# Optimization experiments

Measured on AMD Instinct MI355X. Metric: run time of the kernel, lower is better.

The kernel has to match this reference:

```python
import jax, jax.numpy as jnp
import numpy as np

N_NODES = 100000
N_EDGES = 3200000
N_GRAPHS = 5000
N_LAYERS = 2
BN_EPS = 1e-5


def setup_inputs() -> dict:
    key = jax.random.key(0)
    ks = jax.random.split(key, 20)
    inp = {}
    inp['x'] = jax.random.normal(ks[0], (N_NODES, 14), dtype=jnp.float32)
    inp['edge_index'] = jax.random.randint(ks[1], (2, N_EDGES), 0, N_NODES, dtype=jnp.int64)
    inp['edge_attr'] = jax.random.uniform(ks[2], (N_EDGES, 3), dtype=jnp.float32)
    inp['batch'] = jnp.sort(jax.random.randint(ks[3], (N_NODES,), 0, N_GRAPHS, dtype=jnp.int64))
    s = 0.1
    inp['node_w'] = jax.random.normal(ks[4], (14, 32), dtype=jnp.float32) * s
    inp['node_b'] = jnp.zeros((32,), dtype=jnp.float32)
    inp['edge_w'] = jax.random.normal(ks[5], (3, 32), dtype=jnp.float32) * s
    inp['edge_b'] = jnp.zeros((32,), dtype=jnp.float32)
    inp['conv_w1'] = jax.random.normal(ks[6], (N_LAYERS, 32, 75), dtype=jnp.float32) * s
    inp['conv_b1'] = jnp.zeros((N_LAYERS, 75), dtype=jnp.float32)
    inp['conv_w2'] = jax.random.normal(ks[7], (N_LAYERS, 75, 32), dtype=jnp.float32) * s
    inp['conv_b2'] = jnp.zeros((N_LAYERS, 32), dtype=jnp.float32)
    inp['bn_g'] = jnp.ones((N_LAYERS, 32), dtype=jnp.float32)
    inp['bn_b'] = jnp.zeros((N_LAYERS, 32), dtype=jnp.float32)
    inp['lin1_w'] = jax.random.normal(ks[8], (32, 16), dtype=jnp.float32) * s
    inp['lin1_b'] = jnp.zeros((16,), dtype=jnp.float32)
    inp['lin2_w'] = jax.random.normal(ks[9], (16, 2), dtype=jnp.float32) * s
    inp['lin2_b'] = jnp.zeros((2,), dtype=jnp.float32)
    return inp


def _forward(x, edge_attr, node_w, node_b, edge_w, edge_b,
             conv_w1, conv_b1, conv_w2, conv_b2, bn_g, bn_b,
             lin1_w, lin1_b, lin2_w, lin2_b, edge_index, batch):
    src, dst = edge_index[0], edge_index[1]
    h = x @ node_w + node_b                      # [N, 32]
    ea = edge_attr @ edge_w + edge_b             # [E, 32]
    for l in range(N_LAYERS):
        # GINEConv (eps=0): nn(x_i + sum_j relu(x_j + e_ji))
        msg = jax.nn.relu(h[src] + ea)           # [E, 32]
        agg = jax.ops.segment_sum(msg, dst, num_segments=N_NODES)
        z = h + agg
        z = jax.nn.relu(z @ conv_w1[l] + conv_b1[l]) @ conv_w2[l] + conv_b2[l]
        # BatchNorm1d (training-mode batch statistics)
        mu = jnp.mean(z, axis=0)
        var = jnp.var(z, axis=0)
        z = (z - mu) * jax.lax.rsqrt(var + BN_EPS) * bn_g[l] + bn_b[l]
        h = jax.nn.relu(z)
    # global_mean_pool
    sums = jax.ops.segment_sum(h, batch, num_segments=N_GRAPHS)   # [G, 32]
    counts = jax.ops.segment_sum(jnp.ones((h.shape[0],), h.dtype), batch, num_segments=N_GRAPHS)
    graph_x = sums / jnp.maximum(counts, 1.0)[:, None]
    pred = jax.nn.relu(graph_x @ lin1_w + lin1_b) @ lin2_w + lin2_b  # [G, 2]
    return pred


def reference(x, edge_index, edge_attr, batch, node_w, node_b, edge_w, edge_b,
              conv_w1, conv_b1, conv_w2, conv_b2, bn_g, bn_b,
              lin1_w, lin1_b, lin2_w, lin2_b):
    return _forward(x, edge_attr, node_w, node_b, edge_w, edge_b,
                    conv_w1, conv_b1, conv_w2, conv_b2, bn_g, bn_b,
                    lin1_w, lin1_b, lin2_w, lin2_b, edge_index, batch)
```

## Files before the change

kernel.cpp:

```cpp
#include <hip/hip_runtime.h>
#include <hip/hip_fp16.h>

#define N_NODES 100000
#define N_EDGES 3200000
#define N_GRAPHS 5000
#define BN_EPS 1e-5f
#define HPAD 80
#define CHUNK 2048
#define NBLKA 1563
#define NBKT 196
#define NPAD2 (NBKT * 512)
#define NS1 1197
#define LALLOC (NS1 * 256)
#define VPT 5
#define W1S 36

__global__ void k_encode(const float* __restrict__ x, const float* __restrict__ W,
                         const float* __restrict__ b, float* __restrict__ h,
                         __half* __restrict__ h16) {
    __shared__ float sW[448];
    __shared__ float sb[32];
    for (int i = threadIdx.x; i < 448; i += 256) sW[i] = W[i];
    if (threadIdx.x < 32) sb[threadIdx.x] = b[threadIdx.x];
    __syncthreads();
    int n = blockIdx.x * 256 + threadIdx.x;
    if (n >= N_NODES) return;
    float xi[14];
#pragma unroll
    for (int k = 0; k < 14; k++) xi[k] = x[n * 14 + k];
    float4* hp = (float4*)(h + (size_t)n * 32);
    __half2* hq = (__half2*)(h16 + (size_t)n * 32);
#pragma unroll
    for (int q = 0; q < 8; q++) {
        float4 acc;
        float* ap = (float*)&acc;
#pragma unroll
        for (int i = 0; i < 4; i++) {
            int c = q * 4 + i;
            float a = sb[c];
#pragma unroll
            for (int k = 0; k < 14; k++) a += xi[k] * sW[k * 32 + c];
            ap[i] = a;
        }
        hp[q] = acc;
        hq[q * 2 + 0] = __floats2half2_rn(acc.x, acc.y);
        hq[q * 2 + 1] = __floats2half2_rn(acc.z, acc.w);
    }
}

__global__ void k_prep(const float* __restrict__ W1, const float* __restrict__ b1,
                       const float* __restrict__ W2,
                       float* __restrict__ w1tp, float* __restrict__ b1p,
                       float* __restrict__ w2p) {
    int i = blockIdx.x * 256 + threadIdx.x;
    if (i < 2 * HPAD * 32) {
        int l = i / (HPAD * 32), r = i % (HPAD * 32);
        int j = r / 32, c = r % 32;
        w1tp[i] = (j < 75) ? W1[l * 2400 + c * 75 + j] : 0.f;
        w2p[i]  = (j < 75) ? W2[l * 2400 + j * 32 + c] : 0.f;
    } else if (i < 2 * HPAD * 32 + 2 * HPAD) {
        int k = i - 2 * HPAD * 32;
        int l = k / HPAD, j = k % HPAD;
        b1p[k] = (j < 75) ? b1[l * 75 + j] : 0.f;
    }
}

__global__ void __launch_bounds__(256) ksA(const int* __restrict__ ei, int* __restrict__ cmat) {
    __shared__ int lh[NBKT];
    if (threadIdx.x < NBKT) lh[threadIdx.x] = 0;
    __syncthreads();
    int b0 = blockIdx.x * CHUNK;
    for (int i = threadIdx.x; i < CHUNK; i += 256) {
        int e = b0 + i;
        if (e < N_EDGES) atomicAdd(&lh[ei[N_EDGES + e] >> 9], 1);
    }
    __syncthreads();
    if (threadIdx.x < NBKT) cmat[threadIdx.x * NBLKA + blockIdx.x] = lh[threadIdx.x];
}

__global__ void ks1(const int* __restrict__ a, int* __restrict__ bs) {
    __shared__ int s[256];
    int i = blockIdx.x * 256 + threadIdx.x;
    s[threadIdx.x] = a[i];
    __syncthreads();
    for (int o = 128; o > 0; o >>= 1) {
        if (threadIdx.x < o) s[threadIdx.x] += s[threadIdx.x + o];
        __syncthreads();
    }
    if (threadIdx.x == 0) bs[blockIdx.x] = s[0];
}

__global__ void ks2(int* __restrict__ bs) {
    __shared__ int s[256];
    int t = threadIdx.x;
    int v[VPT];
    int base = t * VPT, sum = 0;
#pragma unroll
    for (int k = 0; k < VPT; k++) {
        int idx = base + k;
        int x = (idx < NS1) ? bs[idx] : 0;
        v[k] = sum; sum += x;
    }
    s[t] = sum;
    __syncthreads();
    for (int o = 1; o < 256; o <<= 1) {
        int add = (t >= o) ? s[t - o] : 0;
        __syncthreads();
        s[t] += add;
        __syncthreads();
    }
    int excl = (t == 0) ? 0 : s[t - 1];
#pragma unroll
    for (int k = 0; k < VPT; k++) {
        int idx = base + k;
        if (idx < NS1) bs[idx] = excl + v[k];
    }
}

__global__ void ks3(int* __restrict__ a, const int* __restrict__ bs) {
    __shared__ int s[256];
    int t = threadIdx.x, i = blockIdx.x * 256 + t;
    int v = a[i];
    s[t] = v;
    __syncthreads();
    for (int o = 1; o < 256; o <<= 1) {
        int add = (t >= o) ? s[t - o] : 0;
        __syncthreads();
        s[t] += add;
        __syncthreads();
    }
    a[i] = s[t] - v + bs[blockIdx.x];
}

__global__ void __launch_bounds__(256) ksB(const int* __restrict__ ei, const float* __restrict__ ea,
                                           const int* __restrict__ cmat, float4* __restrict__ buf1) {
    __shared__ float4 rec[CHUNK];
    __shared__ unsigned short sbkt[CHUNK];
    __shared__ int lh[NBKT];
    __shared__ int lex[NBKT];
    __shared__ int gb[NBKT];
    __shared__ int sc[256];
    int t = threadIdx.x;
    int b0 = blockIdx.x * CHUNK;
    int nval = min(CHUNK, N_EDGES - b0);
    if (t < NBKT) lh[t] = 0;
    __syncthreads();
    for (int i = t; i < nval; i += 256)
        atomicAdd(&lh[ei[N_EDGES + b0 + i] >> 9], 1);
    __syncthreads();
    sc[t] = (t < NBKT) ? lh[t] : 0;
    __syncthreads();
    for (int o = 1; o < 256; o <<= 1) {
        int add = (t >= o) ? sc[t - o] : 0;
        __syncthreads();
        sc[t] += add;
        __syncthreads();
    }
    if (t < NBKT) {
        lex[t] = sc[t] - lh[t];
        gb[t] = cmat[t * NBLKA + blockIdx.x];
        lh[t] = sc[t] - lh[t];
    }
    __syncthreads();
    for (int i = t; i < nval; i += 256) {
        int e = b0 + i;
        int src = ei[e], dst = ei[N_EDGES + e];
        float a0 = ea[(size_t)e * 3 + 0], a1 = ea[(size_t)e * 3 + 1], a2 = ea[(size_t)e * 3 + 2];
        int bkt = dst >> 9;
        int r = atomicAdd(&lh[bkt], 1);
        rec[r] = make_float4(a0, a1, a2, __int_as_float(src | ((dst & 511) << 17)));
        sbkt[r] = (unsigned short)bkt;
    }
    __syncthreads();
    for (int p = t; p < nval; p += 256) {
        int bkt = sbkt[p];
        buf1[gb[bkt] + (p - lex[bkt])] = rec[p];
    }
}

__global__ void __launch_bounds__(1024) ksC(const int* __restrict__ cmat, const float4* __restrict__ buf1,
                                            float4* __restrict__ packed, int* __restrict__ offs) {
    __shared__ int cnt[512];
    __shared__ int sc[512];
    __shared__ int excl[513];
    int g = blockIdx.x, t = threadIdx.x;
    int bb = cmat[g * NBLKA];
    int be = (g == NBKT - 1) ? N_EDGES : cmat[(g + 1) * NBLKA];
    if (t < 512) cnt[t] = 0;
    __syncthreads();
    for (int j = bb + t; j < be; j += 1024) {
        int bits = __float_as_int(buf1[j].w);
        atomicAdd(&cnt[bits >> 17], 1);
    }
    __syncthreads();
    if (t < 512) sc[t] = cnt[t];
    __syncthreads();
    for (int o = 1; o < 512; o <<= 1) {
        int add = 0;
        if (t < 512 && t >= o) add = sc[t - o];
        __syncthreads();
        if (t < 512) sc[t] += add;
        __syncthreads();
    }
    if (t < 512) excl[t] = sc[t] - cnt[t];
    if (t == 511) excl[512] = sc[511];
    __syncthreads();
    if (t < 512) offs[g * 512 + t] = bb + excl[t];
    if (g == NBKT - 1 && t == 0) offs[NPAD2] = N_EDGES;
    if (t < 512) cnt[t] = 0;
    __syncthreads();
    for (int j = bb + t; j < be; j += 1024) {
        float4 r = buf1[j];
        int bits = __float_as_int(r.w);
        int dl = bits >> 17, src = bits & 0x1FFFF;
        int rank = atomicAdd(&cnt[dl], 1);
        packed[bb + excl[dl] + rank] = make_float4(r.x, r.y, r.z, __int_as_float(src));
    }
}

__global__ void __launch_bounds__(256) k_agg(const float4* __restrict__ packed,
                                             const int* __restrict__ offs,
                                             const float* __restrict__ eW, const float* __restrict__ eb,
                                             const __half* __restrict__ h16,
                                             const float* __restrict__ h, float* __restrict__ zin) {
    int t = blockIdx.x * 256 + threadIdx.x;
    int n = t >> 5, s = t & 31;
    int q = s & 7, part = s >> 3;
    int c0 = q * 4;
    float w0[4], w1[4], w2[4], bb4[4];
#pragma unroll
    for (int i = 0; i < 4; i++) {
        w0[i] = eW[c0 + i];
        w1[i] = eW[32 + c0 + i];
        w2[i] = eW[64 + c0 + i];
        bb4[i] = eb[c0 + i];
    }
    int beg = offs[n], end = offs[n + 1];
    float acc0[4] = {0.f, 0.f, 0.f, 0.f};
    float acc1[4] = {0.f, 0.f, 0.f, 0.f};
    int j = beg + part;
    for (; j + 4 < end; j += 8) {
        float4 pa = packed[j];
        float4 pb = packed[j + 4];
        float2 ra = *(const float2*)(h16 + (size_t)__float_as_int(pa.w) * 32 + c0);
        float2 rb = *(const float2*)(h16 + (size_t)__float_as_int(pb.w) * 32 + c0);
        float2 a01 = __half22float2(*(__half2*)&ra.x);
        float2 a23 = __half22float2(*(__half2*)&ra.y);
        float2 b01 = __half22float2(*(__half2*)&rb.x);
        float2 b23 = __half22float2(*(__half2*)&rb.y);
        float ha4[4] = {a01.x, a01.y, a23.x, a23.y};
        float hb4[4] = {b01.x, b01.y, b23.x, b23.y};
#pragma unroll
        for (int i = 0; i < 4; i++) {
            acc0[i] += fmaxf(ha4[i] + pa.x * w0[i] + pa.y * w1[i] + pa.z * w2[i] + bb4[i], 0.f);
            acc1[i] += fmaxf(hb4[i] + pb.x * w0[i] + pb.y * w1[i] + pb.z * w2[i] + bb4[i], 0.f);
        }
    }
    if (j < end) {
        float4 p = packed[j];
        float2 r = *(const float2*)(h16 + (size_t)__float_as_int(p.w) * 32 + c0);
        float2 a01 = __half22float2(*(__half2*)&r.x);
        float2 a23 = __half22float2(*(__half2*)&r.y);
        float hp4[4] = {a01.x, a01.y, a23.x, a23.y};
#pragma unroll
        for (int i = 0; i < 4; i++)
            acc0[i] += fmaxf(hp4[i] + p.x * w0[i] + p.y * w1[i] + p.z * w2[i] + bb4[i], 0.f);
    }
    float acc[4];
#pragma unroll
    for (int i = 0; i < 4; i++) {
        acc[i] = acc0[i] + acc1[i];
        acc[i] += __shfl_xor(acc[i], 8, 64);
        acc[i] += __shfl_xor(acc[i], 16, 64);
    }
    if (part == 0) {
        float4 hq = *(const float4*)(h + (size_t)n * 32 + c0);
        *(float4*)(zin + (size_t)n * 32 + c0) =
            make_float4(acc[0] + hq.x, acc[1] + hq.y, acc[2] + hq.z, acc[3] + hq.w);
    }
}

__global__ void __launch_bounds__(256, 4) k_mlp(float* __restrict__ zio,
                                                const float* __restrict__ W1, const float* __restrict__ B1,
                                                const float* __restrict__ W2, const float* __restrict__ b2) {
    __shared__ float sW1[HPAD * W1S];
    __shared__ float sW2[2560];
    __shared__ float sB1[80];
    __shared__ float sb2[32];
    __shared__ float hidL[32 * 84];
    for (int i = threadIdx.x; i < 2560; i += 256) {
        int j = i >> 5, c = i & 31;
        sW1[j * W1S + c] = W1[i];
        sW2[i] = W2[i];
    }
    if (threadIdx.x < 80) sB1[threadIdx.x] = B1[threadIdx.x];
    if (threadIdx.x < 32) sb2[threadIdx.x] = b2[threadIdx.x];
    __syncthreads();
    unsigned t = blockIdx.x * 256 + threadIdx.x;
    unsigned lane = threadIdx.x & 63;
    unsigned wv = threadIdx.x >> 6;
    unsigned oct = lane >> 3;
    unsigned nd = lane & 7;
    unsigned n = (t >> 6) * 8 + nd;
    const float4* ap = (const float4*)(zio + (size_t)n * 32);
    float zc[32];
#pragma unroll
    for (int q = 0; q < 8; q++) {
        float4 av = ap[q];
        zc[q * 4 + 0] = av.x;
        zc[q * 4 + 1] = av.y;
        zc[q * 4 + 2] = av.z;
        zc[q * 4 + 3] = av.w;
    }
    float hid[10];
#pragma unroll
    for (int i = 0; i < 10; i++) {
        int j = (int)oct * 10 + i;
        const float4* wp = (const float4*)(sW1 + j * W1S);
        float a0 = 0.f, a1 = 0.f, a2 = 0.f, a3 = 0.f;
#pragma unroll
        for (int q = 0; q < 8; q++) {
            float4 wv4 = wp[q];
            a0 += zc[q * 4 + 0] * wv4.x;
            a1 += zc[q * 4 + 1] * wv4.y;
            a2 += zc[q * 4 + 2] * wv4.z;
            a3 += zc[q * 4 + 3] * wv4.w;
        }
        hid[i] = fmaxf(sB1[j] + ((a0 + a1) + (a2 + a3)), 0.f);
    }
    float* hrow = &hidL[(wv * 8 + nd) * 84];
#pragma unroll
    for (int i = 0; i < 10; i++) hrow[oct * 10 + i] = hid[i];
    float4 zo = *(const float4*)(sb2 + oct * 4);
    const float4* hv4 = (const float4*)hrow;
#pragma unroll
    for (int k = 0; k < 20; k++) {
        float4 hv = hv4[k];
        const float* wr = sW2 + (k * 4) * 32 + oct * 4;
        float4 wa = *(const float4*)(wr);
        float4 wb = *(const float4*)(wr + 32);
        float4 wc = *(const float4*)(wr + 64);
        float4 wd = *(const float4*)(wr + 96);
        zo.x += hv.x * wa.x + hv.y * wb.x + hv.z * wc.x + hv.w * wd.x;
        zo.y += hv.x * wa.y + hv.y * wb.y + hv.z * wc.y + hv.w * wd.y;
        zo.z += hv.x * wa.z + hv.y * wb.z + hv.z * wc.z + hv.w * wd.z;
        zo.w += hv.x * wa.w + hv.y * wb.w + hv.z * wc.w + hv.w * wd.w;
    }
    *(float4*)(zio + (size_t)n * 32 + oct * 4) = zo;
}

__global__ void __launch_bounds__(256) k_stats(const float* __restrict__ z, float* __restrict__ stats) {
    __shared__ float ls[4 * 64];
    int tid = threadIdx.x;
    int c = tid & 31;
    float s = 0.f, s2 = 0.f;
    for (int e = blockIdx.x * 256 + tid; e < N_NODES * 32; e += 256 * 256) {
        float v = z[e];
        s += v; s2 += v * v;
    }
    s += __shfl_down(s, 32, 64);
    s2 += __shfl_down(s2, 32, 64);
    int wave = tid >> 6, lane = tid & 63;
    if (lane < 32) { ls[wave * 64 + c] = s; ls[wave * 64 + 32 + c] = s2; }
    __syncthreads();
    if (tid < 64) {
        float a = ls[tid] + ls[64 + tid] + ls[128 + tid] + ls[192 + tid];
        atomicAdd(&stats[tid], a);
    }
}

__global__ void k_bn(const float* __restrict__ z, float* __restrict__ h,
                     __half* __restrict__ h16,
                     const float* __restrict__ stats, const float* __restrict__ g,
                     const float* __restrict__ b) {
    int t = blockIdx.x * 256 + threadIdx.x;
    if (t >= N_NODES * 8) return;
    int q = t & 7;
    float4 zv = ((const float4*)z)[t];
    float* zp = (float*)&zv;
    float4 ov;
    float* op = (float*)&ov;
    const float invN = 1.0f / (float)N_NODES;
#pragma unroll
    for (int i = 0; i < 4; i++) {
        int c = q * 4 + i;
        float mu = stats[c] * invN;
        float var = stats[32 + c] * invN - mu * mu;
        float sc = g[c] / sqrtf(var + BN_EPS);
        op[i] = fmaxf((zp[i] - mu) * sc + b[c], 0.f);
    }
    ((float4*)h)[t] = ov;
    __half2 p0 = __floats2half2_rn(ov.x, ov.y);
    __half2 p1 = __floats2half2_rn(ov.z, ov.w);
    __half2* hq = (__half2*)(h16 + (size_t)t * 4);
    hq[0] = p0;
    hq[1] = p1;
}

__global__ void k_goff(const int* __restrict__ batch, int* __restrict__ goff) {
    int g = blockIdx.x * 256 + threadIdx.x;
    if (g > N_GRAPHS) return;
    int lo = 0, hi = N_NODES;
    while (lo < hi) {
        int mid = (lo + hi) >> 1;
        if (batch[mid] < g) lo = mid + 1; else hi = mid;
    }
    goff[g] = lo;
}

__global__ void __launch_bounds__(256) k_pool2(const float* __restrict__ h, const int* __restrict__ goff,
                                               float* __restrict__ gsum) {
    int wid = threadIdx.x >> 6, lane = threadIdx.x & 63;
    int g = blockIdx.x * 4 + wid;
    if (g >= N_GRAPHS) return;
    int s = goff[g], e = goff[g + 1];
    int c = lane & 31, half = lane >> 5;
    float acc = 0.f;
    for (int n = s + half; n < e; n += 2) acc += h[(size_t)n * 32 + c];
    acc += __shfl_down(acc, 32, 64);
    if (lane < 32) gsum[(size_t)g * 32 + c] = acc;
}

__global__ void k_head(const float* __restrict__ gsum, const int* __restrict__ goff,
                       const float* __restrict__ W1, const float* __restrict__ b1,
                       const float* __restrict__ W2, const float* __restrict__ b2,
                       float* __restrict__ out) {
    __shared__ float sW1[512], sb1[16], sW2[32], sb2[2];
    for (int i = threadIdx.x; i < 512; i += 256) sW1[i] = W1[i];
    if (threadIdx.x < 16) sb1[threadIdx.x] = b1[threadIdx.x];
    if (threadIdx.x < 32) sW2[threadIdx.x] = W2[threadIdx.x];
    if (threadIdx.x < 2) sb2[threadIdx.x] = b2[threadIdx.x];
    __syncthreads();
    int gI = blockIdx.x * 256 + threadIdx.x;
    if (gI >= N_GRAPHS) return;
    float cnt = (float)(goff[gI + 1] - goff[gI]);
    float inv = 1.0f / fmaxf(cnt, 1.0f);
    float gx[32];
#pragma unroll
    for (int c = 0; c < 32; c++) gx[c] = gsum[(size_t)gI * 32 + c] * inv;
    float hid[16];
#pragma unroll
    for (int j = 0; j < 16; j++) {
        float a = sb1[j];
#pragma unroll
        for (int c = 0; c < 32; c++) a += gx[c] * sW1[c * 16 + j];
        hid[j] = fmaxf(a, 0.f);
    }
#pragma unroll
    for (int o = 0; o < 2; o++) {
        float a = sb2[o];
#pragma unroll
        for (int j = 0; j < 16; j++) a += hid[j] * sW2[j * 2 + o];
        out[(size_t)gI * 2 + o] = a;
    }
}

extern "C" void kernel_launch(void* const* d_in, const int* in_sizes, int n_in,
                              void* d_out, int out_size, void* d_ws, size_t ws_size,
                              hipStream_t stream) {
    const float* x       = (const float*)d_in[0];
    const int*   ei      = (const int*)d_in[1];
    const float* eattr   = (const float*)d_in[2];
    const int*   batch   = (const int*)d_in[3];
    const float* node_w  = (const float*)d_in[4];
    const float* node_b  = (const float*)d_in[5];
    const float* edge_w  = (const float*)d_in[6];
    const float* edge_b  = (const float*)d_in[7];
    const float* conv_w1 = (const float*)d_in[8];
    const float* conv_b1 = (const float*)d_in[9];
    const float* conv_w2 = (const float*)d_in[10];
    const float* conv_b2 = (const float*)d_in[11];
    const float* bn_g    = (const float*)d_in[12];
    const float* bn_b    = (const float*)d_in[13];
    const float* lin1_w  = (const float*)d_in[14];
    const float* lin1_b  = (const float*)d_in[15];
    const float* lin2_w  = (const float*)d_in[16];
    const float* lin2_b  = (const float*)d_in[17];
    float* out = (float*)d_out;

    float4* packed = (float4*)d_ws;
    float4* buf1   = packed + N_EDGES;
    float*  h      = (float*)(buf1 + N_EDGES);
    float*  agg    = h + (size_t)N_NODES * 32;
    __half* h16    = (__half*)(agg + (size_t)N_NODES * 32);
    int*    cmat   = (int*)(h16 + (size_t)N_NODES * 32);
    int*    t1     = cmat + LALLOC;
    int*    offs   = t1 + 1280;
    int*    goff   = offs + NPAD2 + 1;
    float*  stats  = (float*)(goff + N_GRAPHS + 1);
    float*  gsum   = stats + 64;
    float*  w1tp   = gsum + (size_t)N_GRAPHS * 32;
    float*  b1p    = w1tp + 2 * HPAD * 32;
    float*  w2p    = b1p + 2 * HPAD;

    int nb_nodes = (N_NODES + 255) / 256;
    int nb_vec   = (N_NODES * 8 + 255) / 256;

    hipMemsetAsync(cmat, 0, LALLOC * sizeof(int), stream);
    k_encode<<<nb_nodes, 256, 0, stream>>>(x, node_w, node_b, h, h16);
    k_prep<<<(2 * HPAD * 32 + 2 * HPAD + 255) / 256, 256, 0, stream>>>(
        conv_w1, conv_b1, conv_w2, w1tp, b1p, w2p);
    k_goff<<<(N_GRAPHS + 1 + 255) / 256, 256, 0, stream>>>(batch, goff);

    ksA<<<NBLKA, 256, 0, stream>>>(ei, cmat);
    ks1<<<NS1, 256, 0, stream>>>(cmat, t1);
    ks2<<<1, 256, 0, stream>>>(t1);
    ks3<<<NS1, 256, 0, stream>>>(cmat, t1);
    ksB<<<NBLKA, 256, 0, stream>>>(ei, eattr, cmat, buf1);
    ksC<<<NBKT, 1024, 0, stream>>>(cmat, buf1, packed, offs);

    for (int l = 0; l < 2; l++) {
        hipMemsetAsync(stats, 0, 64 * sizeof(float), stream);
        k_agg<<<N_NODES * 32 / 256, 256, 0, stream>>>(packed, offs, edge_w, edge_b, h16, h, agg);
        k_mlp<<<N_NODES * 8 / 256, 256, 0, stream>>>(agg, w1tp + l * HPAD * 32,
                                                     b1p + l * HPAD, w2p + l * HPAD * 32,
                                                     conv_b2 + l * 32);
        k_stats<<<256, 256, 0, stream>>>(agg, stats);
        k_bn<<<nb_vec, 256, 0, stream>>>(agg, h, h16, stats, bn_g + l * 32, bn_b + l * 32);
    }
    k_pool2<<<(N_GRAPHS + 3) / 4, 256, 0, stream>>>(h, goff, gsum);
    k_head<<<(N_GRAPHS + 255) / 256, 256, 0, stream>>>(gsum, goff, lin1_w, lin1_b, lin2_w, lin2_b, out);
}
```

Before: 471.1 us.

## Replace two-level edge sort with coarse buckets and shared-memory atomic aggregation

Switches the destination bucketing from 512-node to 128-node buckets and drops the second-level per-node sort kernel (ksC) and its offsets array. Aggregation now runs one block per bucket, accumulating messages into a padded shared-memory tile with LDS float atomics before adding h and writing out. It also skips the fp16 copy of h after the last layer, since nothing reads it. This removes a full pass over the 3.2M edge records. The cost is atomic contention in shared memory, only 782 aggregation blocks, and a float summation order that is no longer deterministic.

Result: slower. 1.688 ms (+258.2%).

```diff
diff --git a/kernel.cpp b/kernel.cpp
--- a/kernel.cpp
+++ b/kernel.cpp
@@ -8,11 +8,11 @@
 #define HPAD 80
 #define CHUNK 2048
 #define NBLKA 1563
-#define NBKT 196
-#define NPAD2 (NBKT * 512)
-#define NS1 1197
+#define NBKT 782
+#define LROW 33
+#define NS1 4775
 #define LALLOC (NS1 * 256)
-#define VPT 5
+#define VPT 19
 #define W1S 36
 
 __global__ void k_encode(const float* __restrict__ x, const float* __restrict__ W,
@@ -67,15 +67,16 @@
 
 __global__ void __launch_bounds__(256) ksA(const int* __restrict__ ei, int* __restrict__ cmat) {
     __shared__ int lh[NBKT];
-    if (threadIdx.x < NBKT) lh[threadIdx.x] = 0;
+    for (int i = threadIdx.x; i < NBKT; i += 256) lh[i] = 0;
     __syncthreads();
     int b0 = blockIdx.x * CHUNK;
     for (int i = threadIdx.x; i < CHUNK; i += 256) {
         int e = b0 + i;
-        if (e < N_EDGES) atomicAdd(&lh[ei[N_EDGES + e] >> 9], 1);
-    }
-    __syncthreads();
-    if (threadIdx.x < NBKT) cmat[threadIdx.x * NBLKA + blockIdx.x] = lh[threadIdx.x];
+        if (e < N_EDGES) atomicAdd(&lh[ei[N_EDGES + e] >> 7], 1);
+    }
+    __syncthreads();
+    for (int i = threadIdx.x; i < NBKT; i += 256)
+        cmat[i * NBLKA + blockIdx.x] = lh[i];
 }
 
 __global__ void ks1(const int* __restrict__ a, int* __restrict__ bs) {
@@ -143,12 +144,19 @@
     int t = threadIdx.x;
     int b0 = blockIdx.x * CHUNK;
     int nval = min(CHUNK, N_EDGES - b0);
-    if (t < NBKT) lh[t] = 0;
+    for (int i = t; i < NBKT; i += 256) lh[i] = 0;
     __syncthreads();
     for (int i = t; i < nval; i += 256)
-        atomicAdd(&lh[ei[N_EDGES + b0 + i] >> 9], 1);
-    __syncthreads();
-    sc[t] = (t < NBKT) ? lh[t] : 0;
+        atomicAdd(&lh[ei[N_EDGES + b0 + i] >> 7], 1);
+    __syncthreads();
+    int v[4]; int run = 0;
+#pragma unroll
+    for (int k = 0; k < 4; k++) {
+        int idx = t * 4 + k;
+        int x = (idx < NBKT) ? lh[idx] : 0;
+        v[k] = run; run += x;
+    }
+    sc[t] = run;
     __syncthreads();
     for (int o = 1; o < 256; o <<= 1) {
         int add = (t >= o) ? sc[t - o] : 0;
@@ -156,19 +164,25 @@
         sc[t] += add;
         __syncthreads();
     }
-    if (t < NBKT) {
-        lex[t] = sc[t] - lh[t];
-        gb[t] = cmat[t * NBLKA + blockIdx.x];
-        lh[t] = sc[t] - lh[t];
+    int excl = (t == 0) ? 0 : sc[t - 1];
+#pragma unroll
+    for (int k = 0; k < 4; k++) {
+        int idx = t * 4 + k;
+        if (idx < NBKT) {
+            int base = excl + v[k];
+            lex[idx] = base;
+            lh[idx] = base;
+            gb[idx] = cmat[idx * NBLKA + blockIdx.x];
+        }
     }
     __syncthreads();
     for (int i = t; i < nval; i += 256) {
         int e = b0 + i;
         int src = ei[e], dst = ei[N_EDGES + e];
         float a0 = ea[(size_t)e * 3 + 0], a1 = ea[(size_t)e * 3 + 1], a2 = ea[(size_t)e * 3 + 2];
-        int bkt = dst >> 9;
+        int bkt = dst >> 7;
         int r = atomicAdd(&lh[bkt], 1);
-        rec[r] = make_float4(a0, a1, a2, __int_as_float(src | ((dst & 511) << 17)));
+        rec[r] = make_float4(a0, a1, a2, __int_as_float(src | ((dst & 127) << 17)));
         sbkt[r] = (unsigned short)bkt;
     }
     __syncthreads();
@@ -178,54 +192,16 @@
     }
 }
 
-__global__ void __launch_bounds__(1024) ksC(const int* __restrict__ cmat, const float4* __restrict__ buf1,
-                                            float4* __restrict__ packed, int* __restrict__ offs) {
-    __shared__ int cnt[512];
-    __shared__ int sc[512];
-    __shared__ int excl[513];
-    int g = blockIdx.x, t = threadIdx.x;
-    int bb = cmat[g * NBLKA];
-    int be = (g == NBKT - 1) ? N_EDGES : cmat[(g + 1) * NBLKA];
-    if (t < 512) cnt[t] = 0;
-    __syncthreads();
-    for (int j = bb + t; j < be; j += 1024) {
-        int bits = __float_as_int(buf1[j].w);
-        atomicAdd(&cnt[bits >> 17], 1);
-    }
-    __syncthreads();
-    if (t < 512) sc[t] = cnt[t];
-    __syncthreads();
-    for (int o = 1; o < 512; o <<= 1) {
-        int add = 0;
-        if (t < 512 && t >= o) add = sc[t - o];
-        __syncthreads();
-        if (t < 512) sc[t] += add;
-        __syncthreads();
-    }
-    if (t < 512) excl[t] = sc[t] - cnt[t];
-    if (t == 511) excl[512] = sc[511];
-    __syncthreads();
-    if (t < 512) offs[g * 512 + t] = bb + excl[t];
-    if (g == NBKT - 1 && t == 0) offs[NPAD2] = N_EDGES;
-    if (t < 512) cnt[t] = 0;
-    __syncthreads();
-    for (int j = bb + t; j < be; j += 1024) {
-        float4 r = buf1[j];
-        int bits = __float_as_int(r.w);
-        int dl = bits >> 17, src = bits & 0x1FFFF;
-        int rank = atomicAdd(&cnt[dl], 1);
-        packed[bb + excl[dl] + rank] = make_float4(r.x, r.y, r.z, __int_as_float(src));
-    }
-}
-
-__global__ void __launch_bounds__(256) k_agg(const float4* __restrict__ packed,
-                                             const int* __restrict__ offs,
-                                             const float* __restrict__ eW, const float* __restrict__ eb,
-                                             const __half* __restrict__ h16,
-                                             const float* __restrict__ h, float* __restrict__ zin) {
-    int t = blockIdx.x * 256 + threadIdx.x;
-    int n = t >> 5, s = t & 31;
-    int q = s & 7, part = s >> 3;
+__global__ void __launch_bounds__(256) k_aggB(const int* __restrict__ cmat,
+                                              const float4* __restrict__ buf1,
+                                              const float* __restrict__ eW, const float* __restrict__ eb,
+                                              const __half* __restrict__ h16,
+                                              const float* __restrict__ h, float* __restrict__ zin) {
+    __shared__ float acc[128 * LROW];
+    int t = threadIdx.x;
+    int g = blockIdx.x;
+    for (int i = t; i < 128 * LROW; i += 256) acc[i] = 0.f;
+    int q = t & 7, er = t >> 3;
     int c0 = q * 4;
     float w0[4], w1[4], w2[4], bb4[4];
 #pragma unroll
@@ -235,48 +211,57 @@
         w2[i] = eW[64 + c0 + i];
         bb4[i] = eb[c0 + i];
     }
-    int beg = offs[n], end = offs[n + 1];
-    float acc0[4] = {0.f, 0.f, 0.f, 0.f};
-    float acc1[4] = {0.f, 0.f, 0.f, 0.f};
-    int j = beg + part;
-    for (; j + 4 < end; j += 8) {
-        float4 pa = packed[j];
-        float4 pb = packed[j + 4];
-        float2 ra = *(const float2*)(h16 + (size_t)__float_as_int(pa.w) * 32 + c0);
-        float2 rb = *(const float2*)(h16 + (size_t)__float_as_int(pb.w) * 32 + c0);
+    int bb = cmat[g * NBLKA];
+    int be = (g == NBKT - 1) ? N_EDGES : cmat[(g + 1) * NBLKA];
+    __syncthreads();
+    int j = bb + er;
+    for (; j + 32 < be; j += 64) {
+        float4 pa = buf1[j];
+        float4 pb = buf1[j + 32];
+        int ba = __float_as_int(pa.w), bbts = __float_as_int(pb.w);
+        float2 ra = *(const float2*)(h16 + (size_t)(ba & 0x1FFFF) * 32 + c0);
+        float2 rb = *(const float2*)(h16 + (size_t)(bbts & 0x1FFFF) * 32 + c0);
         float2 a01 = __half22float2(*(__half2*)&ra.x);
         float2 a23 = __half22float2(*(__half2*)&ra.y);
         float2 b01 = __half22float2(*(__half2*)&rb.x);
         float2 b23 = __half22float2(*(__half2*)&rb.y);
         float ha4[4] = {a01.x, a01.y, a23.x, a23.y};
         float hb4[4] = {b01.x, b01.y, b23.x, b23.y};
+        int da = (ba >> 17) * LROW + c0;
+        int db = (bbts >> 17) * LROW + c0;
 #pragma unroll
         for (int i = 0; i < 4; i++) {
-            acc0[i] += fmaxf(ha4[i] + pa.x * w0[i] + pa.y * w1[i] + pa.z * w2[i] + bb4[i], 0.f);
-            acc1[i] += fmaxf(hb4[i] + pb.x * w0[i] + pb.y * w1[i] + pb.z * w2[i] + bb4[i], 0.f);
+            float ma = fmaxf(ha4[i] + pa.x * w0[i] + pa.y * w1[i] + pa.z * w2[i] + bb4[i], 0.f);
+            float mb = fmaxf(hb4[i] + pb.x * w0[i] + pb.y * w1[i] + pb.z * w2[i] + bb4[i], 0.f);
+            atomicAdd(&acc[da + i], ma);
+            atomicAdd(&acc[db + i], mb);
         }
     }
-    if (j < end) {
-        float4 p = packed[j];
-        float2 r = *(const float2*)(h16 + (size_t)__float_as_int(p.w) * 32 + c0);
+    if (j < be) {
+        float4 p = buf1[j];
+        int bits = __float_as_int(p.w);
+        float2 r = *(const float2*)(h16 + (size_t)(bits & 0x1FFFF) * 32 + c0);
         float2 a01 = __half22float2(*(__half2*)&r.x);
         float2 a23 = __half22float2(*(__half2*)&r.y);
         float hp4[4] = {a01.x, a01.y, a23.x, a23.y};
-#pragma unroll
-        for (int i = 0; i < 4; i++)
-            acc0[i] += fmaxf(hp4[i] + p.x * w0[i] + p.y * w1[i] + p.z * w2[i] + bb4[i], 0.f);
-    }
-    float acc[4];
-#pragma unroll
-    for (int i = 0; i < 4; i++) {
-        acc[i] = acc0[i] + acc1[i];
-        acc[i] += __shfl_xor(acc[i], 8, 64);
-        acc[i] += __shfl_xor(acc[i], 16, 64);
-    }
-    if (part == 0) {
-        float4 hq = *(const float4*)(h + (size_t)n * 32 + c0);
-        *(float4*)(zin + (size_t)n * 32 + c0) =
-            make_float4(acc[0] + hq.x, acc[1] + hq.y, acc[2] + hq.z, acc[3] + hq.w);
+        int d = (bits >> 17) * LROW + c0;
+#pragma unroll
+        for (int i = 0; i < 4; i++) {
+            float m = fmaxf(hp4[i] + p.x * w0[i] + p.y * w1[i] + p.z * w2[i] + bb4[i], 0.f);
+            atomicAdd(&acc[d + i], m);
+        }
+    }
+    __syncthreads();
+    int n0 = g << 7;
+    for (int idx = t; idx < 128 * 8; idx += 256) {
+        int ln = idx >> 3, qq = idx & 7;
+        int n = n0 + ln;
+        if (n < N_NODES) {
+            const float* ap = &acc[ln * LROW + qq * 4];
+            float4 hv = *(const float4*)(h + (size_t)n * 32 + qq * 4);
+            *(float4*)(zin + (size_t)n * 32 + qq * 4) =
+                make_float4(ap[0] + hv.x, ap[1] + hv.y, ap[2] + hv.z, ap[3] + hv.w);
+        }
     }
 }
 
@@ -372,7 +357,7 @@
 __global__ void k_bn(const float* __restrict__ z, float* __restrict__ h,
                      __half* __restrict__ h16,
                      const float* __restrict__ stats, const float* __restrict__ g,
-                     const float* __restrict__ b) {
+                     const float* __restrict__ b, int write16) {
     int t = blockIdx.x * 256 + threadIdx.x;
     if (t >= N_NODES * 8) return;
     int q = t & 7;
@@ -390,11 +375,13 @@
         op[i] = fmaxf((zp[i] - mu) * sc + b[c], 0.f);
     }
     ((float4*)h)[t] = ov;
-    __half2 p0 = __floats2half2_rn(ov.x, ov.y);
-    __half2 p1 = __floats2half2_rn(ov.z, ov.w);
-    __half2* hq = (__half2*)(h16 + (size_t)t * 4);
-    hq[0] = p0;
-    hq[1] = p1;
+    if (write16) {
+        __half2 p0 = __floats2half2_rn(ov.x, ov.y);
+        __half2 p1 = __floats2half2_rn(ov.z, ov.w);
+        __half2* hq = (__half2*)(h16 + (size_t)t * 4);
+        hq[0] = p0;
+        hq[1] = p1;
+    }
 }
 
 __global__ void k_goff(const int* __restrict__ batch, int* __restrict__ goff) {
@@ -478,15 +465,13 @@
     const float* lin2_b  = (const float*)d_in[17];
     float* out = (float*)d_out;
 
-    float4* packed = (float4*)d_ws;
-    float4* buf1   = packed + N_EDGES;
+    float4* buf1   = (float4*)d_ws;
     float*  h      = (float*)(buf1 + N_EDGES);
     float*  agg    = h + (size_t)N_NODES * 32;
     __half* h16    = (__half*)(agg + (size_t)N_NODES * 32);
     int*    cmat   = (int*)(h16 + (size_t)N_NODES * 32);
     int*    t1     = cmat + LALLOC;
-    int*    offs   = t1 + 1280;
-    int*    goff   = offs + NPAD2 + 1;
+    int*    goff   = t1 + 4864;
     float*  stats  = (float*)(goff + N_GRAPHS + 1);
     float*  gsum   = stats + 64;
     float*  w1tp   = gsum + (size_t)N_GRAPHS * 32;
@@ -507,16 +492,16 @@
     ks2<<<1, 256, 0, stream>>>(t1);
     ks3<<<NS1, 256, 0, stream>>>(cmat, t1);
     ksB<<<NBLKA, 256, 0, stream>>>(ei, eattr, cmat, buf1);
-    ksC<<<NBKT, 1024, 0, stream>>>(cmat, buf1, packed, offs);
 
     for (int l = 0; l < 2; l++) {
         hipMemsetAsync(stats, 0, 64 * sizeof(float), stream);
-        k_agg<<<N_NODES * 32 / 256, 256, 0, stream>>>(packed, offs, edge_w, edge_b, h16, h, agg);
+        k_aggB<<<NBKT, 256, 0, stream>>>(cmat, buf1, edge_w, edge_b, h16, h, agg);
         k_mlp<<<N_NODES * 8 / 256, 256, 0, stream>>>(agg, w1tp + l * HPAD * 32,
                                                      b1p + l * HPAD, w2p + l * HPAD * 32,
                                                      conv_b2 + l * 32);
         k_stats<<<256, 256, 0, stream>>>(agg, stats);
-        k_bn<<<nb_vec, 256, 0, stream>>>(agg, h, h16, stats, bn_g + l * 32, bn_b + l * 32);
+        k_bn<<<nb_vec, 256, 0, stream>>>(agg, h, h16, stats, bn_g + l * 32, bn_b + l * 32,
+                                         l == 0 ? 1 : 0);
     }
     k_pool2<<<(N_GRAPHS + 3) / 4, 256, 0, stream>>>(h, goff, gsum);
     k_head<<<(N_GRAPHS + 255) / 256, 256, 0, stream>>>(gsum, goff, lin1_w, lin1_b, lin2_w, lin2_b, out);
```

## Fuse BN stats into MLP, fold BN into agg/pool, atomic-cursor edge placement

Applied to the files above, without the earlier changes.

Computes BatchNorm sums inside the MLP kernel via shuffles and atomics and drops the separate stats pass. BN normalisation is folded into the next layer's aggregation self-term and into the pooling kernel, so the fp32 h tensor is no longer rewritten. The per-bucket counting sort is replaced by per-node degree counts, a global scan and an atomic-cursor scatter, which makes within-node edge order nondeterministic. The aggregation loop is also unrolled to four edges per step for more memory-level parallelism.

Measured after the change: 746.4 us. 58.4% more time.

```diff
diff --git a/kernel.cpp b/kernel.cpp
--- a/kernel.cpp
+++ b/kernel.cpp
@@ -11,9 +11,10 @@
 #define NBKT 196
 #define NPAD2 (NBKT * 512)
 #define NS1 1197
+#define NSB 392
 #define LALLOC (NS1 * 256)
-#define VPT 5
 #define W1S 36
+#define PSLICE 16
 
 __global__ void k_encode(const float* __restrict__ x, const float* __restrict__ W,
                          const float* __restrict__ b, float* __restrict__ h,
@@ -65,14 +66,19 @@
     }
 }
 
-__global__ void __launch_bounds__(256) ksA(const int* __restrict__ ei, int* __restrict__ cmat) {
+__global__ void __launch_bounds__(256) ksA(const int* __restrict__ ei, int* __restrict__ cmat,
+                                           int* __restrict__ nodeCnt) {
     __shared__ int lh[NBKT];
     if (threadIdx.x < NBKT) lh[threadIdx.x] = 0;
     __syncthreads();
     int b0 = blockIdx.x * CHUNK;
     for (int i = threadIdx.x; i < CHUNK; i += 256) {
         int e = b0 + i;
-        if (e < N_EDGES) atomicAdd(&lh[ei[N_EDGES + e] >> 9], 1);
+        if (e < N_EDGES) {
+            int d = ei[N_EDGES + e];
+            atomicAdd(&lh[d >> 9], 1);
+            atomicAdd(&nodeCnt[d], 1);
+        }
     }
     __syncthreads();
     if (threadIdx.x < NBKT) cmat[threadIdx.x * NBLKA + blockIdx.x] = lh[threadIdx.x];
@@ -90,15 +96,16 @@
     if (threadIdx.x == 0) bs[blockIdx.x] = s[0];
 }
 
+template<int NSX, int VPTX>
 __global__ void ks2(int* __restrict__ bs) {
     __shared__ int s[256];
     int t = threadIdx.x;
-    int v[VPT];
-    int base = t * VPT, sum = 0;
-#pragma unroll
-    for (int k = 0; k < VPT; k++) {
+    int v[VPTX];
+    int base = t * VPTX, sum = 0;
+#pragma unroll
+    for (int k = 0; k < VPTX; k++) {
         int idx = base + k;
-        int x = (idx < NS1) ? bs[idx] : 0;
+        int x = (idx < NSX) ? bs[idx] : 0;
         v[k] = sum; sum += x;
     }
     s[t] = sum;
@@ -111,13 +118,13 @@
     }
     int excl = (t == 0) ? 0 : s[t - 1];
 #pragma unroll
-    for (int k = 0; k < VPT; k++) {
+    for (int k = 0; k < VPTX; k++) {
         int idx = base + k;
-        if (idx < NS1) bs[idx] = excl + v[k];
-    }
-}
-
-__global__ void ks3(int* __restrict__ a, const int* __restrict__ bs) {
+        if (idx < NSX) bs[idx] = excl + v[k];
+    }
+}
+
+__global__ void ks3(int* __restrict__ a, const int* __restrict__ bs, int* __restrict__ dup) {
     __shared__ int s[256];
     int t = threadIdx.x, i = blockIdx.x * 256 + t;
     int v = a[i];
@@ -129,7 +136,9 @@
         s[t] += add;
         __syncthreads();
     }
-    a[i] = s[t] - v + bs[blockIdx.x];
+    int val = s[t] - v + bs[blockIdx.x];
+    a[i] = val;
+    if (dup != nullptr) dup[i] = val;
 }
 
 __global__ void __launch_bounds__(256) ksB(const int* __restrict__ ei, const float* __restrict__ ea,
@@ -178,51 +187,35 @@
     }
 }
 
-__global__ void __launch_bounds__(1024) ksC(const int* __restrict__ cmat, const float4* __restrict__ buf1,
-                                            float4* __restrict__ packed, int* __restrict__ offs) {
-    __shared__ int cnt[512];
-    __shared__ int sc[512];
-    __shared__ int excl[513];
-    int g = blockIdx.x, t = threadIdx.x;
+__global__ void __launch_bounds__(256) k_place(const int* __restrict__ cmat,
+                                               const float4* __restrict__ buf1,
+                                               int* __restrict__ cursor,
+                                               float4* __restrict__ packed) {
+    int g = blockIdx.x >> 4, sl = blockIdx.x & (PSLICE - 1);
     int bb = cmat[g * NBLKA];
     int be = (g == NBKT - 1) ? N_EDGES : cmat[(g + 1) * NBLKA];
-    if (t < 512) cnt[t] = 0;
-    __syncthreads();
-    for (int j = bb + t; j < be; j += 1024) {
-        int bits = __float_as_int(buf1[j].w);
-        atomicAdd(&cnt[bits >> 17], 1);
-    }
-    __syncthreads();
-    if (t < 512) sc[t] = cnt[t];
-    __syncthreads();
-    for (int o = 1; o < 512; o <<= 1) {
-        int add = 0;
-        if (t < 512 && t >= o) add = sc[t - o];
-        __syncthreads();
-        if (t < 512) sc[t] += add;
-        __syncthreads();
-    }
-    if (t < 512) excl[t] = sc[t] - cnt[t];
-    if (t == 511) excl[512] = sc[511];
-    __syncthreads();
-    if (t < 512) offs[g * 512 + t] = bb + excl[t];
-    if (g == NBKT - 1 && t == 0) offs[NPAD2] = N_EDGES;
-    if (t < 512) cnt[t] = 0;
-    __syncthreads();
-    for (int j = bb + t; j < be; j += 1024) {
+    int len = be - bb;
+    int ch = (len + PSLICE - 1) >> 4;
+    int s0 = bb + sl * ch;
+    int e0 = min(s0 + ch, be);
+    for (int j = s0 + (int)threadIdx.x; j < e0; j += 256) {
         float4 r = buf1[j];
         int bits = __float_as_int(r.w);
-        int dl = bits >> 17, src = bits & 0x1FFFF;
-        int rank = atomicAdd(&cnt[dl], 1);
-        packed[bb + excl[dl] + rank] = make_float4(r.x, r.y, r.z, __int_as_float(src));
-    }
-}
-
+        int nn = (g << 9) + (bits >> 17);
+        int pos = atomicAdd(&cursor[nn], 1);
+        packed[pos] = make_float4(r.x, r.y, r.z, __int_as_float(bits & 0x1FFFF));
+    }
+}
+
+template<bool BN>
 __global__ void __launch_bounds__(256) k_agg(const float4* __restrict__ packed,
                                              const int* __restrict__ offs,
                                              const float* __restrict__ eW, const float* __restrict__ eb,
                                              const __half* __restrict__ h16,
-                                             const float* __restrict__ h, float* __restrict__ zin) {
+                                             const float* __restrict__ hs,
+                                             const float* __restrict__ stats,
+                                             const float* __restrict__ bng, const float* __restrict__ bnb,
+                                             float* __restrict__ zin) {
     int t = blockIdx.x * 256 + threadIdx.x;
     int n = t >> 5, s = t & 31;
     int q = s & 7, part = s >> 3;
@@ -239,24 +232,36 @@
     float acc0[4] = {0.f, 0.f, 0.f, 0.f};
     float acc1[4] = {0.f, 0.f, 0.f, 0.f};
     int j = beg + part;
-    for (; j + 4 < end; j += 8) {
+    for (; j + 12 < end; j += 16) {
         float4 pa = packed[j];
         float4 pb = packed[j + 4];
+        float4 pc = packed[j + 8];
+        float4 pd = packed[j + 12];
         float2 ra = *(const float2*)(h16 + (size_t)__float_as_int(pa.w) * 32 + c0);
         float2 rb = *(const float2*)(h16 + (size_t)__float_as_int(pb.w) * 32 + c0);
+        float2 rc = *(const float2*)(h16 + (size_t)__float_as_int(pc.w) * 32 + c0);
+        float2 rd = *(const float2*)(h16 + (size_t)__float_as_int(pd.w) * 32 + c0);
         float2 a01 = __half22float2(*(__half2*)&ra.x);
         float2 a23 = __half22float2(*(__half2*)&ra.y);
         float2 b01 = __half22float2(*(__half2*)&rb.x);
         float2 b23 = __half22float2(*(__half2*)&rb.y);
+        float2 c01 = __half22float2(*(__half2*)&rc.x);
+        float2 c23 = __half22float2(*(__half2*)&rc.y);
+        float2 d01 = __half22float2(*(__half2*)&rd.x);
+        float2 d23 = __half22float2(*(__half2*)&rd.y);
         float ha4[4] = {a01.x, a01.y, a23.x, a23.y};
         float hb4[4] = {b01.x, b01.y, b23.x, b23.y};
+        float hc4[4] = {c01.x, c01.y, c23.x, c23.y};
+        float hd4[4] = {d01.x, d01.y, d23.x, d23.y};
 #pragma unroll
         for (int i = 0; i < 4; i++) {
             acc0[i] += fmaxf(ha4[i] + pa.x * w0[i] + pa.y * w1[i] + pa.z * w2[i] + bb4[i], 0.f);
             acc1[i] += fmaxf(hb4[i] + pb.x * w0[i] + pb.y * w1[i] + pb.z * w2[i] + bb4[i], 0.f);
+            acc0[i] += fmaxf(hc4[i] + pc.x * w0[i] + pc.y * w1[i] + pc.z * w2[i] + bb4[i], 0.f);
+            acc1[i] += fmaxf(hd4[i] + pd.x * w0[i] + pd.y * w1[i] + pd.z * w2[i] + bb4[i], 0.f);
         }
     }
-    if (j < end) {
+    for (; j < end; j += 4) {
         float4 p = packed[j];
         float2 r = *(const float2*)(h16 + (size_t)__float_as_int(p.w) * 32 + c0);
         float2 a01 = __half22float2(*(__half2*)&r.x);
@@ -274,20 +279,40 @@
         acc[i] += __shfl_xor(acc[i], 16, 64);
     }
     if (part == 0) {
-        float4 hq = *(const float4*)(h + (size_t)n * 32 + c0);
+        float4 hq = *(const float4*)(hs + (size_t)n * 32 + c0);
+        float* hp = (float*)&hq;
+        float sv[4];
+        if (BN) {
+            const float invN = 1.0f / (float)N_NODES;
+#pragma unroll
+            for (int i = 0; i < 4; i++) {
+                int c = c0 + i;
+                float mu = stats[c] * invN;
+                float var = stats[32 + c] * invN - mu * mu;
+                float scl = bng[c] / sqrtf(var + BN_EPS);
+                float sft = bnb[c] - mu * scl;
+                sv[i] = fmaxf(hp[i] * scl + sft, 0.f);
+            }
+        } else {
+#pragma unroll
+            for (int i = 0; i < 4; i++) sv[i] = hp[i];
+        }
         *(float4*)(zin + (size_t)n * 32 + c0) =
-            make_float4(acc[0] + hq.x, acc[1] + hq.y, acc[2] + hq.z, acc[3] + hq.w);
+            make_float4(acc[0] + sv[0], acc[1] + sv[1], acc[2] + sv[2], acc[3] + sv[3]);
     }
 }
 
 __global__ void __launch_bounds__(256, 4) k_mlp(float* __restrict__ zio,
                                                 const float* __restrict__ W1, const float* __restrict__ B1,
-                                                const float* __restrict__ W2, const float* __restrict__ b2) {
+                                                const float* __restrict__ W2, const float* __restrict__ b2,
+                                                float* __restrict__ stats) {
     __shared__ float sW1[HPAD * W1S];
     __shared__ float sW2[2560];
     __shared__ float sB1[80];
     __shared__ float sb2[32];
     __shared__ float hidL[32 * 84];
+    __shared__ float lsum[128];
+    __shared__ float lsq[128];
     for (int i = threadIdx.x; i < 2560; i += 256) {
         int j = i >> 5, c = i & 31;
         sW1[j * W1S + c] = W1[i];
@@ -347,39 +372,41 @@
         zo.w += hv.x * wa.w + hv.y * wb.w + hv.z * wc.w + hv.w * wd.w;
     }
     *(float4*)(zio + (size_t)n * 32 + oct * 4) = zo;
-}
-
-__global__ void __launch_bounds__(256) k_stats(const float* __restrict__ z, float* __restrict__ stats) {
-    __shared__ float ls[4 * 64];
-    int tid = threadIdx.x;
-    int c = tid & 31;
-    float s = 0.f, s2 = 0.f;
-    for (int e = blockIdx.x * 256 + tid; e < N_NODES * 32; e += 256 * 256) {
-        float v = z[e];
-        s += v; s2 += v * v;
-    }
-    s += __shfl_down(s, 32, 64);
-    s2 += __shfl_down(s2, 32, 64);
-    int wave = tid >> 6, lane = tid & 63;
-    if (lane < 32) { ls[wave * 64 + c] = s; ls[wave * 64 + 32 + c] = s2; }
-    __syncthreads();
-    if (tid < 64) {
-        float a = ls[tid] + ls[64 + tid] + ls[128 + tid] + ls[192 + tid];
-        atomicAdd(&stats[tid], a);
-    }
-}
-
-__global__ void k_bn(const float* __restrict__ z, float* __restrict__ h,
-                     __half* __restrict__ h16,
-                     const float* __restrict__ stats, const float* __restrict__ g,
-                     const float* __restrict__ b) {
+    float s0 = zo.x, s1 = zo.y, s2 = zo.z, s3 = zo.w;
+    float q0 = zo.x * zo.x, q1 = zo.y * zo.y, q2 = zo.z * zo.z, q3 = zo.w * zo.w;
+#pragma unroll
+    for (int m = 1; m < 8; m <<= 1) {
+        s0 += __shfl_xor(s0, m, 64); s1 += __shfl_xor(s1, m, 64);
+        s2 += __shfl_xor(s2, m, 64); s3 += __shfl_xor(s3, m, 64);
+        q0 += __shfl_xor(q0, m, 64); q1 += __shfl_xor(q1, m, 64);
+        q2 += __shfl_xor(q2, m, 64); q3 += __shfl_xor(q3, m, 64);
+    }
+    if (nd == 0) {
+        int base = wv * 32 + oct * 4;
+        lsum[base + 0] = s0; lsum[base + 1] = s1; lsum[base + 2] = s2; lsum[base + 3] = s3;
+        lsq[base + 0] = q0;  lsq[base + 1] = q1;  lsq[base + 2] = q2;  lsq[base + 3] = q3;
+    }
+    __syncthreads();
+    if (threadIdx.x < 32) {
+        int c = threadIdx.x;
+        float tot = lsum[c] + lsum[32 + c] + lsum[64 + c] + lsum[96 + c];
+        atomicAdd(&stats[c], tot);
+    } else if (threadIdx.x < 64) {
+        int c = threadIdx.x - 32;
+        float tot = lsq[c] + lsq[32 + c] + lsq[64 + c] + lsq[96 + c];
+        atomicAdd(&stats[32 + c], tot);
+    }
+}
+
+__global__ void k_bnh(const float* __restrict__ z, __half* __restrict__ m,
+                      const float* __restrict__ stats, const float* __restrict__ g,
+                      const float* __restrict__ b) {
     int t = blockIdx.x * 256 + threadIdx.x;
     if (t >= N_NODES * 8) return;
     int q = t & 7;
     float4 zv = ((const float4*)z)[t];
     float* zp = (float*)&zv;
-    float4 ov;
-    float* op = (float*)&ov;
+    float ov[4];
     const float invN = 1.0f / (float)N_NODES;
 #pragma unroll
     for (int i = 0; i < 4; i++) {
@@ -387,14 +414,11 @@
         float mu = stats[c] * invN;
         float var = stats[32 + c] * invN - mu * mu;
         float sc = g[c] / sqrtf(var + BN_EPS);
-        op[i] = fmaxf((zp[i] - mu) * sc + b[c], 0.f);
-    }
-    ((float4*)h)[t] = ov;
-    __half2 p0 = __floats2half2_rn(ov.x, ov.y);
-    __half2 p1 = __floats2half2_rn(ov.z, ov.w);
-    __half2* hq = (__half2*)(h16 + (size_t)t * 4);
-    hq[0] = p0;
-    hq[1] = p1;
+        ov[i] = fmaxf((zp[i] - mu) * sc + b[c], 0.f);
+    }
+    __half2* hq = (__half2*)(m + (size_t)t * 4);
+    hq[0] = __floats2half2_rn(ov[0], ov[1]);
+    hq[1] = __floats2half2_rn(ov[2], ov[3]);
 }
 
 __global__ void k_goff(const int* __restrict__ batch, int* __restrict__ goff) {
@@ -408,17 +432,25 @@
     goff[g] = lo;
 }
 
-__global__ void __launch_bounds__(256) k_pool2(const float* __restrict__ h, const int* __restrict__ goff,
+__global__ void __launch_bounds__(256) k_pool2(const float* __restrict__ z, const int* __restrict__ goff,
+                                               const float* __restrict__ stats,
+                                               const float* __restrict__ g, const float* __restrict__ b,
                                                float* __restrict__ gsum) {
     int wid = threadIdx.x >> 6, lane = threadIdx.x & 63;
-    int g = blockIdx.x * 4 + wid;
-    if (g >= N_GRAPHS) return;
-    int s = goff[g], e = goff[g + 1];
+    int gi = blockIdx.x * 4 + wid;
+    if (gi >= N_GRAPHS) return;
+    int s = goff[gi], e = goff[gi + 1];
     int c = lane & 31, half = lane >> 5;
+    const float invN = 1.0f / (float)N_NODES;
+    float mu = stats[c] * invN;
+    float var = stats[32 + c] * invN - mu * mu;
+    float scl = g[c] / sqrtf(var + BN_EPS);
+    float sft = b[c] - mu * scl;
     float acc = 0.f;
-    for (int n = s + half; n < e; n += 2) acc += h[(size_t)n * 32 + c];
+    for (int n = s + half; n < e; n += 2)
+        acc += fmaxf(z[(size_t)n * 32 + c] * scl + sft, 0.f);
     acc += __shfl_down(acc, 32, 64);
-    if (lane < 32) gsum[(size_t)g * 32 + c] = acc;
+    if (lane < 32) gsum[(size_t)gi * 32 + c] = acc;
 }
 
 __global__ void k_head(const float* __restrict__ gsum, const int* __restrict__ goff,
@@ -478,46 +510,51 @@
     const float* lin2_b  = (const float*)d_in[17];
     float* out = (float*)d_out;
 
-    float4* packed = (float4*)d_ws;
-    float4* buf1   = packed + N_EDGES;
-    float*  h      = (float*)(buf1 + N_EDGES);
-    float*  agg    = h + (size_t)N_NODES * 32;
-    __half* h16    = (__half*)(agg + (size_t)N_NODES * 32);
-    int*    cmat   = (int*)(h16 + (size_t)N_NODES * 32);
-    int*    t1     = cmat + LALLOC;
-    int*    offs   = t1 + 1280;
-    int*    goff   = offs + NPAD2 + 1;
-    float*  stats  = (float*)(goff + N_GRAPHS + 1);
-    float*  gsum   = stats + 64;
-    float*  w1tp   = gsum + (size_t)N_GRAPHS * 32;
-    float*  b1p    = w1tp + 2 * HPAD * 32;
-    float*  w2p    = b1p + 2 * HPAD;
+    float4* buf1    = (float4*)d_ws;
+    float4* packed  = buf1 + N_EDGES;
+    float*  h       = (float*)(packed + N_EDGES);
+    float*  agg     = h + (size_t)N_NODES * 32;
+    __half* m16     = (__half*)(agg + (size_t)N_NODES * 32);
+    int*    cmat    = (int*)(m16 + (size_t)N_NODES * 32);
+    int*    nodeCnt = cmat + LALLOC;
+    float*  stats   = (float*)(nodeCnt + NPAD2);
+    int*    cursor  = (int*)(stats + 128);
+    int*    t1      = cursor + NPAD2;
+    int*    t2      = t1 + 1280;
+    int*    goff    = t2 + 512;
+    float*  gsum    = (float*)(goff + N_GRAPHS + 1);
+    float*  w1tp    = gsum + (size_t)N_GRAPHS * 32;
+    float*  b1p     = w1tp + 2 * HPAD * 32;
+    float*  w2p     = b1p + 2 * HPAD;
 
     int nb_nodes = (N_NODES + 255) / 256;
     int nb_vec   = (N_NODES * 8 + 255) / 256;
 
-    hipMemsetAsync(cmat, 0, LALLOC * sizeof(int), stream);
-    k_encode<<<nb_nodes, 256, 0, stream>>>(x, node_w, node_b, h, h16);
+    hipMemsetAsync(cmat, 0, (size_t)(LALLOC + NPAD2 + 128) * sizeof(int), stream);
+    k_encode<<<nb_nodes, 256, 0, stream>>>(x, node_w, node_b, h, m16);
     k_prep<<<(2 * HPAD * 32 + 2 * HPAD + 255) / 256, 256, 0, stream>>>(
         conv_w1, conv_b1, conv_w2, w1tp, b1p, w2p);
     k_goff<<<(N_GRAPHS + 1 + 255) / 256, 256, 0, stream>>>(batch, goff);
 
-    ksA<<<NBLKA, 256, 0, stream>>>(ei, cmat);
+    ksA<<<NBLKA, 256, 0, stream>>>(ei, cmat, nodeCnt);
     ks1<<<NS1, 256, 0, stream>>>(cmat, t1);
-    ks2<<<1, 256, 0, stream>>>(t1);
-    ks3<<<NS1, 256, 0, stream>>>(cmat, t1);
+    ks2<NS1, 5><<<1, 256, 0, stream>>>(t1);
+    ks3<<<NS1, 256, 0, stream>>>(cmat, t1, nullptr);
+    ks1<<<NSB, 256, 0, stream>>>(nodeCnt, t2);
+    ks2<NSB, 2><<<1, 256, 0, stream>>>(t2);
+    ks3<<<NSB, 256, 0, stream>>>(nodeCnt, t2, cursor);
+
     ksB<<<NBLKA, 256, 0, stream>>>(ei, eattr, cmat, buf1);
-    ksC<<<NBKT, 1024, 0, stream>>>(cmat, buf1, packed, offs);
-
-    for (int l = 0; l < 2; l++) {
-        hipMemsetAsync(stats, 0, 64 * sizeof(float), stream);
-        k_agg<<<N_NODES * 32 / 256, 256, 0, stream>>>(packed, offs, edge_w, edge_b, h16, h, agg);
-        k_mlp<<<N_NODES * 8 / 256, 256, 0, stream>>>(agg, w1tp + l * HPAD * 32,
-                                                     b1p + l * HPAD, w2p + l * HPAD * 32,
-                                                     conv_b2 + l * 32);
-        k_stats<<<256, 256, 0, stream>>>(agg, stats);
-        k_bn<<<nb_vec, 256, 0, stream>>>(agg, h, h16, stats, bn_g + l * 32, bn_b + l * 32);
-    }
-    k_pool2<<<(N_GRAPHS + 3) / 4, 256, 0, stream>>>(h, goff, gsum);
+    k_place<<<NBKT * PSLICE, 256, 0, stream>>>(cmat, buf1, cursor, packed);
+
+    k_agg<false><<<N_NODES * 32 / 256, 256, 0, stream>>>(packed, nodeCnt, edge_w, edge_b,
+                                                         m16, h, stats, bn_g, bn_b, agg);
+    k_mlp<<<N_NODES * 8 / 256, 256, 0, stream>>>(agg, w1tp, b1p, w2p, conv_b2, stats);
+    k_bnh<<<nb_vec, 256, 0, stream>>>(agg, m16, stats, bn_g, bn_b);
+    k_agg<true><<<N_NODES * 32 / 256, 256, 0, stream>>>(packed, nodeCnt, edge_w, edge_b,
+                                                        m16, agg, stats, bn_g, bn_b, h);
+    k_mlp<<<N_NODES * 8 / 256, 256, 0, stream>>>(h, w1tp + HPAD * 32, b1p + HPAD,
+                                                 w2p + HPAD * 32, conv_b2 + 32, stats + 64);
+    k_pool2<<<(N_GRAPHS + 3) / 4, 256, 0, stream>>>(h, goff, stats + 64, bn_g + 32, bn_b + 32, gsum);
     k_head<<<(N_GRAPHS + 255) / 256, 256, 0, stream>>>(gsum, goff, lin1_w, lin1_b, lin2_w, lin2_b, out);
 }
```
